# Kernel optimization log

Measured on AMD Instinct MI355X. Metric: run time of the kernel, lower is better.

## Reference

```python
import jax, jax.numpy as jnp
import numpy as np

B, T, LATENT, D, N_ENVS = 128, 64, 16, 512, 4
TOPK_RATIO = 0.1
TEMPERATURE = 1.0


def setup_inputs() -> dict:
    key = jax.random.key(0)
    k1, k2, k3, k4 = jax.random.split(key, 4)
    z_s = jax.random.normal(k1, (B, T, LATENT), dtype=jnp.float32)
    env_idx = jax.random.randint(k2, (B,), 0, N_ENVS, dtype=jnp.int64 if jax.config.jax_enable_x64 else jnp.int32)
    A_base = jax.random.normal(k3, (D, D), dtype=jnp.float32) * 0.1
    A_deltas = jax.random.normal(k4, (N_ENVS, D, D), dtype=jnp.float32) * 0.01  # stacked ParameterList
    return {"z_s": z_s, "env_idx": env_idx, "A_base": A_base, "A_deltas": A_deltas}


def reference(z_s, env_idx, A_base, A_deltas):
    b = z_s.shape[0]
    d = A_base.shape[0]
    # Per-env delta add: the torch loop sums delta_e * (env_idx==e) over envs,
    # which (one env per sample) equals a gather of A_deltas at env_idx.
    A_logits = A_base[None, :, :] + A_deltas[env_idx]          # [B, d, d]
    A_soft = jax.nn.sigmoid(A_logits / TEMPERATURE)            # [B, d, d]
    # Batched top-k sparsification (replaces the per-sample python loop).
    k = max(1, int(TOPK_RATIO * d * d))
    flat = A_logits.reshape(b, d * d)                          # [B, d*d]
    topk_vals, topk_idx = jax.lax.top_k(flat, k)               # [B, k]
    rows = jnp.arange(b)[:, None]                              # [B, 1]
    A_flat = jnp.zeros_like(flat).at[rows, topk_idx].set(jax.nn.sigmoid(topk_vals))
    A = A_flat.reshape(b, d, d)
    return A, A_logits, A_soft
```

## Files before the change

### kernel.cpp

```cpp
#include <hip/hip_runtime.h>
#include <stdint.h>

#define D_DIM   512
#define DD      262144
#define DD4     65536
#define B_DIM   128
#define N_ENVS  4
#define K_SEL   26214
#define BDD     33554432u
#define NBLK    64
#define CAP2    98304
#define CAP3    4096

typedef float nfloat4 __attribute__((ext_vector_type(4)));

#define PK_OFF      64
#define CNT_OFF     128
#define HISTP_OFF   4096
#define PAIRS_OFF   (512 * 1024)
#define PAIRS_BYTES ((size_t)N_ENVS * CAP2 * 8)
#define SEL_NEED    (PAIRS_OFF + PAIRS_BYTES)

__device__ __forceinline__ uint32_t fkey(float f) {
    uint32_t u = __float_as_uint(f);
    return (u & 0x80000000u) ? ~u : (u | 0x80000000u);
}
__device__ __forceinline__ float sigmoidf_(float x) {
    return 1.0f / (1.0f + __expf(-x));
}

__global__ __launch_bounds__(256) void hist8_kernel(
    const float* __restrict__ base, const float* __restrict__ deltas,
    uint32_t* __restrict__ histp, uint32_t* __restrict__ cnt8)
{
    int e = blockIdx.y;
    const float4* b4 = (const float4*)base;
    const float4* d4 = (const float4*)(deltas + (size_t)e * DD);
    __shared__ uint32_t s_h[256];
    int tid = threadIdx.x;
    s_h[tid] = 0;
    if (blockIdx.x == 0 && tid == 0) cnt8[e] = 0;
    __syncthreads();
    int g0 = blockIdx.x * 256 + tid;
    #pragma unroll
    for (int r = 0; r < 4; ++r) {
        int g = g0 + r * 16384;
        float4 bv = b4[g], dv = d4[g];
        atomicAdd(&s_h[fkey(bv.x + dv.x) >> 24], 1u);
        atomicAdd(&s_h[fkey(bv.y + dv.y) >> 24], 1u);
        atomicAdd(&s_h[fkey(bv.z + dv.z) >> 24], 1u);
        atomicAdd(&s_h[fkey(bv.w + dv.w) >> 24], 1u);
    }
    __syncthreads();
    histp[(blockIdx.x * N_ENVS + e) * 256 + tid] = s_h[tid];
}

__global__ __launch_bounds__(256) void gather8_kernel(
    const float* __restrict__ base, const float* __restrict__ deltas,
    const uint32_t* __restrict__ histp, uint32_t* __restrict__ pk,
    uint32_t* __restrict__ cnt8, uint2* __restrict__ pairs8)
{
    int e = blockIdx.y;
    const float4* b4 = (const float4*)base;
    const float4* d4 = (const float4*)(deltas + (size_t)e * DD);
    uint2* pp = pairs8 + (size_t)e * CAP2;
    __shared__ uint32_t s_h[256];
    __shared__ uint32_t s_scan[256];
    __shared__ uint32_t s_P, s_base;
    int tid = threadIdx.x;

    uint32_t sum = 0;
    #pragma unroll 8
    for (int j = 0; j < NBLK; ++j)
        sum += histp[(j * N_ENVS + e) * 256 + tid];
    s_h[tid] = sum;
    __syncthreads();
    if (tid == 0) {
        uint32_t cum = 0;
        for (int b = 255; b >= 0; --b) {
            uint32_t c = s_h[b];
            if (cum + c >= (uint32_t)K_SEL) {
                s_P = (uint32_t)b;
                if (blockIdx.x == 0) {
                    pk[2 * e + 0] = (uint32_t)b;
                    pk[2 * e + 1] = (uint32_t)K_SEL - cum;
                }
                break;
            }
            cum += c;
        }
    }
    __syncthreads();
    uint32_t P = s_P;

    int g0 = blockIdx.x * 256 + tid;
    uint32_t keys[16];
    uint32_t m = 0;
    #pragma unroll
    for (int r = 0; r < 4; ++r) {
        int g = g0 + r * 16384;
        float4 bv = b4[g], dv = d4[g];
        uint32_t k0 = fkey(bv.x + dv.x), k1 = fkey(bv.y + dv.y);
        uint32_t k2 = fkey(bv.z + dv.z), k3 = fkey(bv.w + dv.w);
        keys[r * 4 + 0] = k0; keys[r * 4 + 1] = k1;
        keys[r * 4 + 2] = k2; keys[r * 4 + 3] = k3;
        m += ((k0 >> 24) == P) + ((k1 >> 24) == P)
           + ((k2 >> 24) == P) + ((k3 >> 24) == P);
    }
    s_scan[tid] = m;
    __syncthreads();
    #pragma unroll
    for (int off = 1; off < 256; off <<= 1) {
        uint32_t v = (tid >= off) ? s_scan[tid - off] : 0u;
        __syncthreads();
        s_scan[tid] += v;
        __syncthreads();
    }
    uint32_t excl = s_scan[tid] - m;
    if (tid == 255) s_base = atomicAdd(&cnt8[e], s_scan[255]);
    __syncthreads();
    uint32_t pos = s_base + excl;

    #pragma unroll
    for (int r = 0; r < 4; ++r) {
        int g = g0 + r * 16384;
        #pragma unroll
        for (int j = 0; j < 4; ++j) {
            uint32_t key = keys[r * 4 + j];
            if ((key >> 24) == P) {
                if (pos < CAP2) pp[pos] = make_uint2(key, (uint32_t)(g * 4 + j));
                ++pos;
            }
        }
    }
}

__global__ __launch_bounds__(1024) void select2_kernel(
    const uint32_t* __restrict__ pk, const uint32_t* __restrict__ cnt8,
    const uint2* __restrict__ pairs8, uint32_t* __restrict__ thrcut)
{
    int e = blockIdx.x;
    const uint2* pp = pairs8 + (size_t)e * CAP2;
    uint32_t M = cnt8[e]; if (M > CAP2) M = CAP2;
    uint32_t krem8 = pk[2 * e + 1];

    __shared__ uint32_t s_h16[256];
    __shared__ uint2    s_pairs[CAP3];
    __shared__ uint32_t s_b16, s_krem16, s_cnt;
    int tid = threadIdx.x;
    if (tid < 256) s_h16[tid] = 0;
    if (tid == 0) s_cnt = 0;
    __syncthreads();

    for (uint32_t j = tid; j < M; j += 1024)
        atomicAdd(&s_h16[(pp[j].x >> 16) & 255u], 1u);
    __syncthreads();
    if (tid == 0) {
        uint32_t cum = 0;
        for (int b = 255; b >= 0; --b) {
            uint32_t c = s_h16[b];
            if (cum + c >= krem8) { s_b16 = (uint32_t)b; s_krem16 = krem8 - cum; break; }
            cum += c;
        }
    }
    __syncthreads();
    uint32_t b16 = s_b16;
    for (uint32_t j = tid; j < M; j += 1024) {
        uint2 p = pp[j];
        if (((p.x >> 16) & 255u) == b16) {
            uint32_t pos = atomicAdd(&s_cnt, 1u);
            if (pos < CAP3) s_pairs[pos] = p;
        }
    }
    __syncthreads();
    uint32_t M2 = s_cnt; if (M2 > CAP3) M2 = CAP3;
    uint32_t target = s_krem16 - 1;
    for (uint32_t j = tid; j < M2; j += 1024) {
        uint2 me = s_pairs[j];
        uint32_t rank = 0;
        for (uint32_t l = 0; l < M2; ++l) {
            uint2 o = s_pairs[l];
            rank += (o.x > me.x) || (o.x == me.x && o.y < me.y);
        }
        if (rank == target) {
            thrcut[2 * e + 0] = me.x;
            thrcut[2 * e + 1] = me.y;
        }
    }
}

__global__ __launch_bounds__(256) void write_bcast_kernel(
    const int* __restrict__ env_idx, const float* __restrict__ base,
    const float* __restrict__ deltas, const uint32_t* __restrict__ thrcut,
    float* __restrict__ out)
{
    int g = blockIdx.x * 256 + threadIdx.x;
    uint32_t i0 = (uint32_t)g * 4u;
    float4 bv = ((const float4*)base)[g];

    nfloat4 lgv[N_ENVS], sgv[N_ENVS], avv[N_ENVS];
    #pragma unroll
    for (int e = 0; e < N_ENVS; ++e) {
        float4 dv = ((const float4*)(deltas + (size_t)e * DD))[g];
        uint32_t T = thrcut[2 * e], C = thrcut[2 * e + 1];
        nfloat4 lg = { bv.x + dv.x, bv.y + dv.y, bv.z + dv.z, bv.w + dv.w };
        nfloat4 sg = { sigmoidf_(lg.x), sigmoidf_(lg.y),
                       sigmoidf_(lg.z), sigmoidf_(lg.w) };
        uint32_t kx = fkey(lg.x), ky = fkey(lg.y);
        uint32_t kz = fkey(lg.z), kw = fkey(lg.w);
        nfloat4 av;
        av.x = (kx > T || (kx == T && i0 + 0u <= C)) ? sg.x : 0.0f;
        av.y = (ky > T || (ky == T && i0 + 1u <= C)) ? sg.y : 0.0f;
        av.z = (kz > T || (kz == T && i0 + 2u <= C)) ? sg.z : 0.0f;
        av.w = (kw > T || (kw == T && i0 + 3u <= C)) ? sg.w : 0.0f;
        lgv[e] = lg; sgv[e] = sg; avv[e] = av;
    }

    const int ROWS = B_DIM / 8;
    int b0 = blockIdx.y * ROWS;
    nfloat4* o0 = (nfloat4*)out + g;
    #pragma unroll 4
    for (int bb = 0; bb < ROWS; ++bb) {
        int b = b0 + bb;
        int e = env_idx[b];
        nfloat4* o = o0 + (size_t)b * DD4;
        switch (e) {
        case 0: o[0] = avv[0]; o[BDD/4] = lgv[0]; o[2*(BDD/4)] = sgv[0]; break;
        case 1: o[0] = avv[1]; o[BDD/4] = lgv[1]; o[2*(BDD/4)] = sgv[1]; break;
        case 2: o[0] = avv[2]; o[BDD/4] = lgv[2]; o[2*(BDD/4)] = sgv[2]; break;
        default: o[0] = avv[3]; o[BDD/4] = lgv[3]; o[2*(BDD/4)] = sgv[3]; break;
        }
    }
}

extern "C" void kernel_launch(void* const* d_in, const int* in_sizes, int n_in,
                              void* d_out, int out_size, void* d_ws, size_t ws_size,
                              hipStream_t stream) {
    const int*   env_idx  = (const int*)d_in[1];
    const float* A_base   = (const float*)d_in[2];
    const float* A_deltas = (const float*)d_in[3];
    float* out = (float*)d_out;

    uint32_t* thrcut = (uint32_t*)d_ws;

    char* scratch;
    if (ws_size >= SEL_NEED) {
        scratch = (char*)d_ws;
    } else {
        size_t out_bytes = (size_t)out_size * sizeof(float);
        scratch = (char*)d_out + ((out_bytes - SEL_NEED) & ~(size_t)255);
    }
    uint32_t* pk     = (uint32_t*)(scratch + PK_OFF);
    uint32_t* cnt8   = (uint32_t*)(scratch + CNT_OFF);
    uint32_t* histp  = (uint32_t*)(scratch + HISTP_OFF);
    uint2*    pairs8 = (uint2*)   (scratch + PAIRS_OFF);

    hist8_kernel  <<<dim3(NBLK, N_ENVS), 256, 0, stream>>>(A_base, A_deltas,
                                                           histp, cnt8);
    gather8_kernel<<<dim3(NBLK, N_ENVS), 256, 0, stream>>>(A_base, A_deltas, histp,
                                                           pk, cnt8, pairs8);
    select2_kernel<<<N_ENVS, 1024, 0, stream>>>(pk, cnt8, pairs8, thrcut);
    write_bcast_kernel<<<dim3(DD4 / 256, 8), 256, 0, stream>>>(
        env_idx, A_base, A_deltas, thrcut, out);
}
```

Measured before the change: 456.3 us.

## Fuse top-k pipeline into one cooperative kernel with early logit/sigmoid writes

Replaces the four-kernel sequence (histogram, gather, select, broadcast write) with a single cooperative kernel that uses grid-wide syncs between phases. The logits and sigmoid output writes, which are two thirds of the output traffic, are moved ahead of the threshold selection so they overlap the radix-select work. Only the sparse A output is written after the threshold is known. This removes launch gaps between kernels, but during the select phase only 4 of 256 blocks are busy. The write phase also has fewer, larger threads than the old broadcast kernel. The old path remains as a fallback if the cooperative launch fails or the workspace is too small.

```diff
diff --git a/kernel.cpp b/kernel.cpp
--- a/kernel.cpp
+++ b/kernel.cpp
@@ -1,5 +1,8 @@
 #include <hip/hip_runtime.h>
+#include <hip/hip_cooperative_groups.h>
 #include <stdint.h>
+
+namespace cg = cooperative_groups;
 
 #define D_DIM   512
 #define DD      262144
@@ -8,6 +11,7 @@
 #define N_ENVS  4
 #define K_SEL   26214
 #define BDD     33554432u
+#define NSLICE  64
 #define NBLK    64
 #define CAP2    98304
 #define CAP3    4096
@@ -27,6 +31,205 @@
 }
 __device__ __forceinline__ float sigmoidf_(float x) {
     return 1.0f / (1.0f + __expf(-x));
+}
+
+__global__ __launch_bounds__(1024) void mega_kernel(
+    const int* __restrict__ env_idx, const float* __restrict__ base,
+    const float* __restrict__ deltas, uint32_t* __restrict__ histp,
+    uint32_t* __restrict__ cnt8, uint2* __restrict__ pairs8,
+    uint32_t* __restrict__ thrcut, float* __restrict__ out)
+{
+    cg::grid_group grid = cg::this_grid();
+    const int bid = blockIdx.x;
+    const int tid = threadIdx.x;
+    const int e   = bid & (N_ENVS - 1);
+    const int s   = bid >> 2;
+
+    __shared__ uint32_t s_h[256];
+    __shared__ uint32_t s_scan[1024];
+    __shared__ uint32_t s_misc[4];
+    __shared__ uint2    s_pairs[CAP3];
+
+    const float4* b4 = (const float4*)base;
+    const float4* d4 = (const float4*)(deltas + (size_t)e * DD);
+
+    if (tid < 256) s_h[tid] = 0;
+    if (s == 0 && tid == 0) cnt8[e] = 0;
+    __syncthreads();
+    const int g_sel = s * 1024 + tid;
+    float4 bs = b4[g_sel], ds = d4[g_sel];
+    uint32_t k0 = fkey(bs.x + ds.x), k1 = fkey(bs.y + ds.y);
+    uint32_t k2 = fkey(bs.z + ds.z), k3 = fkey(bs.w + ds.w);
+    atomicAdd(&s_h[k0 >> 24], 1u);
+    atomicAdd(&s_h[k1 >> 24], 1u);
+    atomicAdd(&s_h[k2 >> 24], 1u);
+    atomicAdd(&s_h[k3 >> 24], 1u);
+    __syncthreads();
+    if (tid < 256) histp[(s * N_ENVS + e) * 256 + tid] = s_h[tid];
+
+    {
+        const int gt = bid * 1024 + tid;
+        const int gq = gt & (DD4 - 1);
+        const int h  = gt >> 16;
+        float4 bq = b4[gq];
+        nfloat4 lgv[N_ENVS], sgv[N_ENVS];
+        #pragma unroll
+        for (int e2 = 0; e2 < N_ENVS; ++e2) {
+            float4 dq = ((const float4*)(deltas + (size_t)e2 * DD))[gq];
+            nfloat4 lg = { bq.x + dq.x, bq.y + dq.y, bq.z + dq.z, bq.w + dq.w };
+            lgv[e2] = lg;
+            sgv[e2] = nfloat4{ sigmoidf_(lg.x), sigmoidf_(lg.y),
+                               sigmoidf_(lg.z), sigmoidf_(lg.w) };
+        }
+        nfloat4* o0 = (nfloat4*)out + gq;
+        #pragma unroll 4
+        for (int bb = 0; bb < 32; ++bb) {
+            int b = h * 32 + bb;
+            int ee = env_idx[b];
+            nfloat4* o = o0 + (size_t)b * DD4;
+            switch (ee) {
+            case 0:  o[BDD/4] = lgv[0]; o[2*(BDD/4)] = sgv[0]; break;
+            case 1:  o[BDD/4] = lgv[1]; o[2*(BDD/4)] = sgv[1]; break;
+            case 2:  o[BDD/4] = lgv[2]; o[2*(BDD/4)] = sgv[2]; break;
+            default: o[BDD/4] = lgv[3]; o[2*(BDD/4)] = sgv[3]; break;
+            }
+        }
+    }
+    grid.sync();
+
+    if (tid < 256) {
+        uint32_t sum = 0;
+        #pragma unroll 8
+        for (int j = 0; j < NSLICE; ++j)
+            sum += histp[(j * N_ENVS + e) * 256 + tid];
+        s_h[tid] = sum;
+    }
+    __syncthreads();
+    if (tid == 0) {
+        uint32_t cum = 0;
+        for (int b = 255; b >= 0; --b) {
+            uint32_t c = s_h[b];
+            if (cum + c >= (uint32_t)K_SEL) {
+                s_misc[0] = (uint32_t)b;
+                s_misc[1] = (uint32_t)K_SEL - cum;
+                break;
+            }
+            cum += c;
+        }
+    }
+    __syncthreads();
+    const uint32_t P = s_misc[0];
+    uint32_t m = ((k0 >> 24) == P) + ((k1 >> 24) == P)
+               + ((k2 >> 24) == P) + ((k3 >> 24) == P);
+    s_scan[tid] = m;
+    __syncthreads();
+    #pragma unroll
+    for (int off = 1; off < 1024; off <<= 1) {
+        uint32_t v = (tid >= off) ? s_scan[tid - off] : 0u;
+        __syncthreads();
+        s_scan[tid] += v;
+        __syncthreads();
+    }
+    uint32_t excl = s_scan[tid] - m;
+    if (tid == 1023) s_misc[2] = atomicAdd(&cnt8[e], s_scan[1023]);
+    __syncthreads();
+    {
+        uint32_t pos = s_misc[2] + excl;
+        uint2* pp = pairs8 + (size_t)e * CAP2;
+        uint32_t kk[4] = { k0, k1, k2, k3 };
+        #pragma unroll
+        for (int j = 0; j < 4; ++j) {
+            if ((kk[j] >> 24) == P) {
+                if (pos < CAP2) pp[pos] = make_uint2(kk[j], (uint32_t)(g_sel * 4 + j));
+                ++pos;
+            }
+        }
+    }
+    grid.sync();
+
+    if (bid < N_ENVS) {
+        const uint2* pp = pairs8 + (size_t)bid * CAP2;
+        uint32_t M = cnt8[bid]; if (M > CAP2) M = CAP2;
+        uint32_t krem8 = s_misc[1];
+        if (tid < 256) s_h[tid] = 0;
+        if (tid == 0) s_misc[3] = 0;
+        __syncthreads();
+        for (uint32_t j = tid; j < M; j += 1024)
+            atomicAdd(&s_h[(pp[j].x >> 16) & 255u], 1u);
+        __syncthreads();
+        if (tid == 0) {
+            uint32_t cum = 0;
+            for (int b = 255; b >= 0; --b) {
+                uint32_t c = s_h[b];
+                if (cum + c >= krem8) { s_misc[0] = (uint32_t)b; s_misc[1] = krem8 - cum; break; }
+                cum += c;
+            }
+        }
+        __syncthreads();
+        uint32_t b16 = s_misc[0];
+        for (uint32_t j = tid; j < M; j += 1024) {
+            uint2 p = pp[j];
+            if (((p.x >> 16) & 255u) == b16) {
+                uint32_t pos = atomicAdd(&s_misc[3], 1u);
+                if (pos < CAP3) s_pairs[pos] = p;
+            }
+        }
+        __syncthreads();
+        uint32_t M2 = s_misc[3]; if (M2 > CAP3) M2 = CAP3;
+        uint32_t target = s_misc[1] - 1;
+        for (uint32_t j = tid; j < M2; j += 1024) {
+            uint2 me = s_pairs[j];
+            uint32_t rank = 0;
+            for (uint32_t l = 0; l < M2; ++l) {
+                uint2 o = s_pairs[l];
+                rank += (o.x > me.x) || (o.x == me.x && o.y < me.y);
+            }
+            if (rank == target) {
+                thrcut[2 * bid + 0] = me.x;
+                thrcut[2 * bid + 1] = me.y;
+            }
+        }
+        __threadfence();
+    }
+    grid.sync();
+
+    {
+        const int gt = bid * 1024 + tid;
+        const int gq = gt & (DD4 - 1);
+        const int h  = gt >> 16;
+        const uint32_t i0 = (uint32_t)gq * 4u;
+        float4 bq = b4[gq];
+        nfloat4 avv[N_ENVS];
+        #pragma unroll
+        for (int e2 = 0; e2 < N_ENVS; ++e2) {
+            float4 dq = ((const float4*)(deltas + (size_t)e2 * DD))[gq];
+            uint32_t T = thrcut[2 * e2], C = thrcut[2 * e2 + 1];
+            nfloat4 lg = { bq.x + dq.x, bq.y + dq.y, bq.z + dq.z, bq.w + dq.w };
+            nfloat4 sg = { sigmoidf_(lg.x), sigmoidf_(lg.y),
+                           sigmoidf_(lg.z), sigmoidf_(lg.w) };
+            uint32_t kx = fkey(lg.x), ky = fkey(lg.y);
+            uint32_t kz = fkey(lg.z), kw = fkey(lg.w);
+            nfloat4 av;
+            av.x = (kx > T || (kx == T && i0 + 0u <= C)) ? sg.x : 0.0f;
+            av.y = (ky > T || (ky == T && i0 + 1u <= C)) ? sg.y : 0.0f;
+            av.z = (kz > T || (kz == T && i0 + 2u <= C)) ? sg.z : 0.0f;
+            av.w = (kw > T || (kw == T && i0 + 3u <= C)) ? sg.w : 0.0f;
+            avv[e2] = av;
+        }
+        nfloat4* o0 = (nfloat4*)out + gq;
+        #pragma unroll 4
+        for (int bb = 0; bb < 32; ++bb) {
+            int b = h * 32 + bb;
+            int ee = env_idx[b];
+            nfloat4* o = o0 + (size_t)b * DD4;
+            switch (ee) {
+            case 0:  o[0] = avv[0]; break;
+            case 1:  o[0] = avv[1]; break;
+            case 2:  o[0] = avv[2]; break;
+            default: o[0] = avv[3]; break;
+            }
+        }
+    }
 }
 
 __global__ __launch_bounds__(256) void hist8_kernel(
@@ -68,7 +271,6 @@
     __shared__ uint32_t s_scan[256];
     __shared__ uint32_t s_P, s_base;
     int tid = threadIdx.x;
-
     uint32_t sum = 0;
     #pragma unroll 8
     for (int j = 0; j < NBLK; ++j)
@@ -92,7 +294,6 @@
     }
     __syncthreads();
     uint32_t P = s_P;
-
     int g0 = blockIdx.x * 256 + tid;
     uint32_t keys[16];
     uint32_t m = 0;
@@ -100,12 +301,10 @@
     for (int r = 0; r < 4; ++r) {
         int g = g0 + r * 16384;
         float4 bv = b4[g], dv = d4[g];
-        uint32_t k0 = fkey(bv.x + dv.x), k1 = fkey(bv.y + dv.y);
-        uint32_t k2 = fkey(bv.z + dv.z), k3 = fkey(bv.w + dv.w);
-        keys[r * 4 + 0] = k0; keys[r * 4 + 1] = k1;
-        keys[r * 4 + 2] = k2; keys[r * 4 + 3] = k3;
-        m += ((k0 >> 24) == P) + ((k1 >> 24) == P)
-           + ((k2 >> 24) == P) + ((k3 >> 24) == P);
+        uint32_t c0 = fkey(bv.x + dv.x), c1 = fkey(bv.y + dv.y);
+        uint32_t c2 = fkey(bv.z + dv.z), c3 = fkey(bv.w + dv.w);
+        keys[r*4+0]=c0; keys[r*4+1]=c1; keys[r*4+2]=c2; keys[r*4+3]=c3;
+        m += ((c0>>24)==P) + ((c1>>24)==P) + ((c2>>24)==P) + ((c3>>24)==P);
     }
     s_scan[tid] = m;
     __syncthreads();
@@ -120,7 +319,6 @@
     if (tid == 255) s_base = atomicAdd(&cnt8[e], s_scan[255]);
     __syncthreads();
     uint32_t pos = s_base + excl;
-
     #pragma unroll
     for (int r = 0; r < 4; ++r) {
         int g = g0 + r * 16384;
@@ -143,7 +341,6 @@
     const uint2* pp = pairs8 + (size_t)e * CAP2;
     uint32_t M = cnt8[e]; if (M > CAP2) M = CAP2;
     uint32_t krem8 = pk[2 * e + 1];
-
     __shared__ uint32_t s_h16[256];
     __shared__ uint2    s_pairs[CAP3];
     __shared__ uint32_t s_b16, s_krem16, s_cnt;
@@ -151,7 +348,6 @@
     if (tid < 256) s_h16[tid] = 0;
     if (tid == 0) s_cnt = 0;
     __syncthreads();
-
     for (uint32_t j = tid; j < M; j += 1024)
         atomicAdd(&s_h16[(pp[j].x >> 16) & 255u], 1u);
     __syncthreads();
@@ -197,7 +393,6 @@
     int g = blockIdx.x * 256 + threadIdx.x;
     uint32_t i0 = (uint32_t)g * 4u;
     float4 bv = ((const float4*)base)[g];
-
     nfloat4 lgv[N_ENVS], sgv[N_ENVS], avv[N_ENVS];
     #pragma unroll
     for (int e = 0; e < N_ENVS; ++e) {
@@ -215,7 +410,6 @@
         av.w = (kw > T || (kw == T && i0 + 3u <= C)) ? sg.w : 0.0f;
         lgv[e] = lg; sgv[e] = sg; avv[e] = av;
     }
-
     const int ROWS = B_DIM / 8;
     int b0 = blockIdx.y * ROWS;
     nfloat4* o0 = (nfloat4*)out + g;
@@ -243,8 +437,9 @@
 
     uint32_t* thrcut = (uint32_t*)d_ws;
 
+    bool ws_ok = (ws_size >= SEL_NEED);
     char* scratch;
-    if (ws_size >= SEL_NEED) {
+    if (ws_ok) {
         scratch = (char*)d_ws;
     } else {
         size_t out_bytes = (size_t)out_size * sizeof(float);
@@ -255,11 +450,24 @@
     uint32_t* histp  = (uint32_t*)(scratch + HISTP_OFF);
     uint2*    pairs8 = (uint2*)   (scratch + PAIRS_OFF);
 
-    hist8_kernel  <<<dim3(NBLK, N_ENVS), 256, 0, stream>>>(A_base, A_deltas,
-                                                           histp, cnt8);
-    gather8_kernel<<<dim3(NBLK, N_ENVS), 256, 0, stream>>>(A_base, A_deltas, histp,
-                                                           pk, cnt8, pairs8);
-    select2_kernel<<<N_ENVS, 1024, 0, stream>>>(pk, cnt8, pairs8, thrcut);
-    write_bcast_kernel<<<dim3(DD4 / 256, 8), 256, 0, stream>>>(
-        env_idx, A_base, A_deltas, thrcut, out);
-}
+    bool launched = false;
+    if (ws_ok) {
+        void* args[] = { (void*)&env_idx, (void*)&A_base, (void*)&A_deltas,
+                         (void*)&histp, (void*)&cnt8, (void*)&pairs8,
+                         (void*)&thrcut, (void*)&out };
+        hipError_t err = hipLaunchCooperativeKernel(
+            (const void*)mega_kernel, dim3(NSLICE * N_ENVS), dim3(1024),
+            args, 0, stream);
+        launched = (err == hipSuccess);
+        if (!launched) (void)hipGetLastError();
+    }
+    if (!launched) {
+        hist8_kernel  <<<dim3(NBLK, N_ENVS), 256, 0, stream>>>(A_base, A_deltas,
+                                                               histp, cnt8);
+        gather8_kernel<<<dim3(NBLK, N_ENVS), 256, 0, stream>>>(A_base, A_deltas,
+                                                               histp, pk, cnt8, pairs8);
+        select2_kernel<<<N_ENVS, 1024, 0, stream>>>(pk, cnt8, pairs8, thrcut);
+        write_bcast_kernel<<<dim3(DD4 / 256, 8), 256, 0, stream>>>(
+            env_idx, A_base, A_deltas, thrcut, out);
+    }
+}
```

Result: slower. 556.7 us (+22.0%).

## Fuse select pass into gather kernel via last-block ticket, cache env_idx in LDS

Applied to the files above, without the earlier changes.

Removes the separate select2 launch. The last block to finish the gather kernel (found with an atomic ticket counter plus threadfences) now does the per-env radix refinement and rank selection for all four envs in sequence. It uses 256 threads instead of four 1024-thread blocks. The write kernel also stages env_idx in shared memory. This saves one kernel launch and its gap, but the selection tail now runs serially on a single block with a quarter of the threads, so it may take longer.

```diff
diff --git a/kernel.cpp b/kernel.cpp
--- a/kernel.cpp
+++ b/kernel.cpp
@@ -16,6 +16,7 @@
 
 #define PK_OFF      64
 #define CNT_OFF     128
+#define TICKET_OFF  144
 #define HISTP_OFF   4096
 #define PAIRS_OFF   (512 * 1024)
 #define PAIRS_BYTES ((size_t)N_ENVS * CAP2 * 8)
@@ -31,7 +32,8 @@
 
 __global__ __launch_bounds__(256) void hist8_kernel(
     const float* __restrict__ base, const float* __restrict__ deltas,
-    uint32_t* __restrict__ histp, uint32_t* __restrict__ cnt8)
+    uint32_t* __restrict__ histp, uint32_t* __restrict__ cnt8,
+    uint32_t* __restrict__ ticket)
 {
     int e = blockIdx.y;
     const float4* b4 = (const float4*)base;
@@ -39,7 +41,10 @@
     __shared__ uint32_t s_h[256];
     int tid = threadIdx.x;
     s_h[tid] = 0;
-    if (blockIdx.x == 0 && tid == 0) cnt8[e] = 0;
+    if (blockIdx.x == 0 && tid == 0) {
+        cnt8[e] = 0;
+        if (e == 0) *ticket = 0;
+    }
     __syncthreads();
     int g0 = blockIdx.x * 256 + tid;
     #pragma unroll
@@ -55,10 +60,11 @@
     histp[(blockIdx.x * N_ENVS + e) * 256 + tid] = s_h[tid];
 }
 
-__global__ __launch_bounds__(256) void gather8_kernel(
+__global__ __launch_bounds__(256) void gather_sel_kernel(
     const float* __restrict__ base, const float* __restrict__ deltas,
     const uint32_t* __restrict__ histp, uint32_t* __restrict__ pk,
-    uint32_t* __restrict__ cnt8, uint2* __restrict__ pairs8)
+    uint32_t* __restrict__ cnt8, uint2* __restrict__ pairs8,
+    uint32_t* __restrict__ ticket, uint32_t* __restrict__ thrcut)
 {
     int e = blockIdx.y;
     const float4* b4 = (const float4*)base;
@@ -66,7 +72,8 @@
     uint2* pp = pairs8 + (size_t)e * CAP2;
     __shared__ uint32_t s_h[256];
     __shared__ uint32_t s_scan[256];
-    __shared__ uint32_t s_P, s_base;
+    __shared__ uint2    s_pairs[CAP3];
+    __shared__ uint32_t s_P, s_base, s_cnt, s_b16, s_krem16, s_last;
     int tid = threadIdx.x;
 
     uint32_t sum = 0;
@@ -100,12 +107,10 @@
     for (int r = 0; r < 4; ++r) {
         int g = g0 + r * 16384;
         float4 bv = b4[g], dv = d4[g];
-        uint32_t k0 = fkey(bv.x + dv.x), k1 = fkey(bv.y + dv.y);
-        uint32_t k2 = fkey(bv.z + dv.z), k3 = fkey(bv.w + dv.w);
-        keys[r * 4 + 0] = k0; keys[r * 4 + 1] = k1;
-        keys[r * 4 + 2] = k2; keys[r * 4 + 3] = k3;
-        m += ((k0 >> 24) == P) + ((k1 >> 24) == P)
-           + ((k2 >> 24) == P) + ((k3 >> 24) == P);
+        uint32_t c0 = fkey(bv.x + dv.x), c1 = fkey(bv.y + dv.y);
+        uint32_t c2 = fkey(bv.z + dv.z), c3 = fkey(bv.w + dv.w);
+        keys[r*4+0]=c0; keys[r*4+1]=c1; keys[r*4+2]=c2; keys[r*4+3]=c3;
+        m += ((c0>>24)==P) + ((c1>>24)==P) + ((c2>>24)==P) + ((c3>>24)==P);
     }
     s_scan[tid] = m;
     __syncthreads();
@@ -133,59 +138,59 @@
             }
         }
     }
-}
-
-__global__ __launch_bounds__(1024) void select2_kernel(
-    const uint32_t* __restrict__ pk, const uint32_t* __restrict__ cnt8,
-    const uint2* __restrict__ pairs8, uint32_t* __restrict__ thrcut)
-{
-    int e = blockIdx.x;
-    const uint2* pp = pairs8 + (size_t)e * CAP2;
-    uint32_t M = cnt8[e]; if (M > CAP2) M = CAP2;
-    uint32_t krem8 = pk[2 * e + 1];
-
-    __shared__ uint32_t s_h16[256];
-    __shared__ uint2    s_pairs[CAP3];
-    __shared__ uint32_t s_b16, s_krem16, s_cnt;
-    int tid = threadIdx.x;
-    if (tid < 256) s_h16[tid] = 0;
-    if (tid == 0) s_cnt = 0;
-    __syncthreads();
-
-    for (uint32_t j = tid; j < M; j += 1024)
-        atomicAdd(&s_h16[(pp[j].x >> 16) & 255u], 1u);
-    __syncthreads();
-    if (tid == 0) {
-        uint32_t cum = 0;
-        for (int b = 255; b >= 0; --b) {
-            uint32_t c = s_h16[b];
-            if (cum + c >= krem8) { s_b16 = (uint32_t)b; s_krem16 = krem8 - cum; break; }
-            cum += c;
-        }
-    }
-    __syncthreads();
-    uint32_t b16 = s_b16;
-    for (uint32_t j = tid; j < M; j += 1024) {
-        uint2 p = pp[j];
-        if (((p.x >> 16) & 255u) == b16) {
-            uint32_t pos = atomicAdd(&s_cnt, 1u);
-            if (pos < CAP3) s_pairs[pos] = p;
-        }
-    }
-    __syncthreads();
-    uint32_t M2 = s_cnt; if (M2 > CAP3) M2 = CAP3;
-    uint32_t target = s_krem16 - 1;
-    for (uint32_t j = tid; j < M2; j += 1024) {
-        uint2 me = s_pairs[j];
-        uint32_t rank = 0;
-        for (uint32_t l = 0; l < M2; ++l) {
-            uint2 o = s_pairs[l];
-            rank += (o.x > me.x) || (o.x == me.x && o.y < me.y);
-        }
-        if (rank == target) {
-            thrcut[2 * e + 0] = me.x;
-            thrcut[2 * e + 1] = me.y;
-        }
+
+    __threadfence();
+    __syncthreads();
+    if (tid == 0)
+        s_last = (atomicAdd(ticket, 1u) == (uint32_t)(NBLK * N_ENVS - 1));
+    __syncthreads();
+    if (!s_last) return;
+    __threadfence();
+
+    for (int e2 = 0; e2 < N_ENVS; ++e2) {
+        const uint2* qq = pairs8 + (size_t)e2 * CAP2;
+        uint32_t M = cnt8[e2]; if (M > CAP2) M = CAP2;
+        uint32_t krem8 = pk[2 * e2 + 1];
+
+        s_h[tid] = 0;
+        if (tid == 0) s_cnt = 0;
+        __syncthreads();
+        for (uint32_t j = tid; j < M; j += 256)
+            atomicAdd(&s_h[(qq[j].x >> 16) & 255u], 1u);
+        __syncthreads();
+        if (tid == 0) {
+            uint32_t cum = 0;
+            for (int b = 255; b >= 0; --b) {
+                uint32_t c = s_h[b];
+                if (cum + c >= krem8) { s_b16 = (uint32_t)b; s_krem16 = krem8 - cum; break; }
+                cum += c;
+            }
+        }
+        __syncthreads();
+        uint32_t b16 = s_b16;
+        for (uint32_t j = tid; j < M; j += 256) {
+            uint2 p = qq[j];
+            if (((p.x >> 16) & 255u) == b16) {
+                uint32_t q = atomicAdd(&s_cnt, 1u);
+                if (q < CAP3) s_pairs[q] = p;
+            }
+        }
+        __syncthreads();
+        uint32_t M2 = s_cnt; if (M2 > CAP3) M2 = CAP3;
+        uint32_t target = s_krem16 - 1;
+        for (uint32_t j = tid; j < M2; j += 256) {
+            uint2 me = s_pairs[j];
+            uint32_t rank = 0;
+            for (uint32_t l = 0; l < M2; ++l) {
+                uint2 o = s_pairs[l];
+                rank += (o.x > me.x) || (o.x == me.x && o.y < me.y);
+            }
+            if (rank == target) {
+                thrcut[2 * e2 + 0] = me.x;
+                thrcut[2 * e2 + 1] = me.y;
+            }
+        }
+        __syncthreads();
     }
 }
 
@@ -194,7 +199,11 @@
     const float* __restrict__ deltas, const uint32_t* __restrict__ thrcut,
     float* __restrict__ out)
 {
-    int g = blockIdx.x * 256 + threadIdx.x;
+    __shared__ int s_env[B_DIM];
+    int tid = threadIdx.x;
+    if (tid < B_DIM) s_env[tid] = env_idx[tid];
+
+    int g = blockIdx.x * 256 + tid;
     uint32_t i0 = (uint32_t)g * 4u;
     float4 bv = ((const float4*)base)[g];
 
@@ -215,6 +224,7 @@
         av.w = (kw > T || (kw == T && i0 + 3u <= C)) ? sg.w : 0.0f;
         lgv[e] = lg; sgv[e] = sg; avv[e] = av;
     }
+    __syncthreads();
 
     const int ROWS = B_DIM / 8;
     int b0 = blockIdx.y * ROWS;
@@ -222,7 +232,7 @@
     #pragma unroll 4
     for (int bb = 0; bb < ROWS; ++bb) {
         int b = b0 + bb;
-        int e = env_idx[b];
+        int e = s_env[b];
         nfloat4* o = o0 + (size_t)b * DD4;
         switch (e) {
         case 0: o[0] = avv[0]; o[BDD/4] = lgv[0]; o[2*(BDD/4)] = sgv[0]; break;
@@ -252,14 +262,14 @@
     }
     uint32_t* pk     = (uint32_t*)(scratch + PK_OFF);
     uint32_t* cnt8   = (uint32_t*)(scratch + CNT_OFF);
+    uint32_t* ticket = (uint32_t*)(scratch + TICKET_OFF);
     uint32_t* histp  = (uint32_t*)(scratch + HISTP_OFF);
     uint2*    pairs8 = (uint2*)   (scratch + PAIRS_OFF);
 
-    hist8_kernel  <<<dim3(NBLK, N_ENVS), 256, 0, stream>>>(A_base, A_deltas,
-                                                           histp, cnt8);
-    gather8_kernel<<<dim3(NBLK, N_ENVS), 256, 0, stream>>>(A_base, A_deltas, histp,
-                                                           pk, cnt8, pairs8);
-    select2_kernel<<<N_ENVS, 1024, 0, stream>>>(pk, cnt8, pairs8, thrcut);
+    hist8_kernel<<<dim3(NBLK, N_ENVS), 256, 0, stream>>>(
+        A_base, A_deltas, histp, cnt8, ticket);
+    gather_sel_kernel<<<dim3(NBLK, N_ENVS), 256, 0, stream>>>(
+        A_base, A_deltas, histp, pk, cnt8, pairs8, ticket, thrcut);
     write_bcast_kernel<<<dim3(DD4 / 256, 8), 256, 0, stream>>>(
         env_idx, A_base, A_deltas, thrcut, out);
 }
```

New measurement: 793.1 us. 1.74x slower.

## Overlap logits/sigmoid plane writes with top-k selection kernels

Applied to the files above, without the earlier changes.

Adds extra blocks to the histogram and gather kernels that write the A_logits and A_soft output planes, so those bandwidth-heavy stores run while the latency-bound selection stages work. The final kernel then writes only the sparse A plane. Env indices are staged in shared memory. When the workspace is too small, the old path is kept, because scratch then aliases the output buffer. The risk is extra contention in the selection kernels, but the total bytes written stay the same.

```diff
diff --git a/kernel.cpp b/kernel.cpp
--- a/kernel.cpp
+++ b/kernel.cpp
@@ -21,6 +21,9 @@
 #define PAIRS_BYTES ((size_t)N_ENVS * CAP2 * 8)
 #define SEL_NEED    (PAIRS_OFF + PAIRS_BYTES)
 
+#define SEL_BLOCKS  (NBLK * N_ENVS)
+#define WR_BLOCKS   1024
+
 __device__ __forceinline__ uint32_t fkey(float f) {
     uint32_t u = __float_as_uint(f);
     return (u & 0x80000000u) ? ~u : (u | 0x80000000u);
@@ -29,109 +32,161 @@
     return 1.0f / (1.0f + __expf(-x));
 }
 
-__global__ __launch_bounds__(256) void hist8_kernel(
-    const float* __restrict__ base, const float* __restrict__ deltas,
-    uint32_t* __restrict__ histp, uint32_t* __restrict__ cnt8)
-{
-    int e = blockIdx.y;
-    const float4* b4 = (const float4*)base;
-    const float4* d4 = (const float4*)(deltas + (size_t)e * DD);
-    __shared__ uint32_t s_h[256];
-    int tid = threadIdx.x;
-    s_h[tid] = 0;
-    if (blockIdx.x == 0 && tid == 0) cnt8[e] = 0;
-    __syncthreads();
-    int g0 = blockIdx.x * 256 + tid;
+__device__ __forceinline__ void write_lgsg_band(
+    const int* __restrict__ env_idx, const float* __restrict__ base,
+    const float* __restrict__ deltas, float* __restrict__ out,
+    int c, int h, int tid)
+{
+    __shared__ int s_env[16];
+    if (tid < 16) s_env[tid] = env_idx[h * 16 + tid];
+    int g = c * 256 + tid;
+    float4 bv = ((const float4*)base)[g];
+    nfloat4 lgv[N_ENVS], sgv[N_ENVS];
     #pragma unroll
-    for (int r = 0; r < 4; ++r) {
-        int g = g0 + r * 16384;
-        float4 bv = b4[g], dv = d4[g];
-        atomicAdd(&s_h[fkey(bv.x + dv.x) >> 24], 1u);
-        atomicAdd(&s_h[fkey(bv.y + dv.y) >> 24], 1u);
-        atomicAdd(&s_h[fkey(bv.z + dv.z) >> 24], 1u);
-        atomicAdd(&s_h[fkey(bv.w + dv.w) >> 24], 1u);
-    }
-    __syncthreads();
-    histp[(blockIdx.x * N_ENVS + e) * 256 + tid] = s_h[tid];
-}
-
-__global__ __launch_bounds__(256) void gather8_kernel(
-    const float* __restrict__ base, const float* __restrict__ deltas,
-    const uint32_t* __restrict__ histp, uint32_t* __restrict__ pk,
-    uint32_t* __restrict__ cnt8, uint2* __restrict__ pairs8)
-{
-    int e = blockIdx.y;
-    const float4* b4 = (const float4*)base;
-    const float4* d4 = (const float4*)(deltas + (size_t)e * DD);
-    uint2* pp = pairs8 + (size_t)e * CAP2;
-    __shared__ uint32_t s_h[256];
-    __shared__ uint32_t s_scan[256];
-    __shared__ uint32_t s_P, s_base;
-    int tid = threadIdx.x;
-
-    uint32_t sum = 0;
-    #pragma unroll 8
-    for (int j = 0; j < NBLK; ++j)
-        sum += histp[(j * N_ENVS + e) * 256 + tid];
-    s_h[tid] = sum;
-    __syncthreads();
-    if (tid == 0) {
-        uint32_t cum = 0;
-        for (int b = 255; b >= 0; --b) {
-            uint32_t c = s_h[b];
-            if (cum + c >= (uint32_t)K_SEL) {
-                s_P = (uint32_t)b;
-                if (blockIdx.x == 0) {
-                    pk[2 * e + 0] = (uint32_t)b;
-                    pk[2 * e + 1] = (uint32_t)K_SEL - cum;
+    for (int e = 0; e < N_ENVS; ++e) {
+        float4 dv = ((const float4*)(deltas + (size_t)e * DD))[g];
+        nfloat4 lg = { bv.x + dv.x, bv.y + dv.y, bv.z + dv.z, bv.w + dv.w };
+        lgv[e] = lg;
+        sgv[e] = nfloat4{ sigmoidf_(lg.x), sigmoidf_(lg.y),
+                          sigmoidf_(lg.z), sigmoidf_(lg.w) };
+    }
+    __syncthreads();
+    nfloat4* o0 = (nfloat4*)out + g;
+    #pragma unroll 4
+    for (int bb = 0; bb < 16; ++bb) {
+        int b = h * 16 + bb;
+        int e = s_env[bb];
+        nfloat4* o = o0 + (size_t)b * DD4;
+        switch (e) {
+        case 0:  o[BDD/4] = lgv[0]; o[2*(BDD/4)] = sgv[0]; break;
+        case 1:  o[BDD/4] = lgv[1]; o[2*(BDD/4)] = sgv[1]; break;
+        case 2:  o[BDD/4] = lgv[2]; o[2*(BDD/4)] = sgv[2]; break;
+        default: o[BDD/4] = lgv[3]; o[2*(BDD/4)] = sgv[3]; break;
+        }
+    }
+}
+
+__global__ __launch_bounds__(256) void k1_hist_lgsg(
+    const int* __restrict__ env_idx, const float* __restrict__ base,
+    const float* __restrict__ deltas, uint32_t* __restrict__ histp,
+    uint32_t* __restrict__ cnt8, float* __restrict__ out)
+{
+    int bid = blockIdx.x;
+    int tid = threadIdx.x;
+    if (bid < SEL_BLOCKS) {
+        int e = bid & (N_ENVS - 1);
+        int s = bid >> 2;
+        const float4* b4 = (const float4*)base;
+        const float4* d4 = (const float4*)(deltas + (size_t)e * DD);
+        __shared__ uint32_t s_h[256];
+        s_h[tid] = 0;
+        if (s == 0 && tid == 0) cnt8[e] = 0;
+        __syncthreads();
+        int g0 = s * 256 + tid;
+        #pragma unroll
+        for (int r = 0; r < 4; ++r) {
+            int g = g0 + r * 16384;
+            float4 bv = b4[g], dv = d4[g];
+            atomicAdd(&s_h[fkey(bv.x + dv.x) >> 24], 1u);
+            atomicAdd(&s_h[fkey(bv.y + dv.y) >> 24], 1u);
+            atomicAdd(&s_h[fkey(bv.z + dv.z) >> 24], 1u);
+            atomicAdd(&s_h[fkey(bv.w + dv.w) >> 24], 1u);
+        }
+        __syncthreads();
+        histp[(s * N_ENVS + e) * 256 + tid] = s_h[tid];
+    } else {
+        int w = bid - SEL_BLOCKS;
+        int c = w & 255;
+        int h = w >> 8;
+        write_lgsg_band(env_idx, base, deltas, out, c, h, tid);
+    }
+}
+
+__global__ __launch_bounds__(256) void k2_gather_lgsg(
+    const int* __restrict__ env_idx, const float* __restrict__ base,
+    const float* __restrict__ deltas, const uint32_t* __restrict__ histp,
+    uint32_t* __restrict__ pk, uint32_t* __restrict__ cnt8,
+    uint2* __restrict__ pairs8, float* __restrict__ out)
+{
+    int bid = blockIdx.x;
+    int tid = threadIdx.x;
+    if (bid < SEL_BLOCKS) {
+        int e = bid & (N_ENVS - 1);
+        int s = bid >> 2;
+        const float4* b4 = (const float4*)base;
+        const float4* d4 = (const float4*)(deltas + (size_t)e * DD);
+        uint2* pp = pairs8 + (size_t)e * CAP2;
+        __shared__ uint32_t s_h[256];
+        __shared__ uint32_t s_scan[256];
+        __shared__ uint32_t s_P, s_base;
+
+        uint32_t sum = 0;
+        #pragma unroll 8
+        for (int j = 0; j < NBLK; ++j)
+            sum += histp[(j * N_ENVS + e) * 256 + tid];
+        s_h[tid] = sum;
+        __syncthreads();
+        if (tid == 0) {
+            uint32_t cum = 0;
+            for (int b = 255; b >= 0; --b) {
+                uint32_t cc = s_h[b];
+                if (cum + cc >= (uint32_t)K_SEL) {
+                    s_P = (uint32_t)b;
+                    if (s == 0) {
+                        pk[2 * e + 0] = (uint32_t)b;
+                        pk[2 * e + 1] = (uint32_t)K_SEL - cum;
+                    }
+                    break;
                 }
-                break;
+                cum += cc;
             }
-            cum += c;
-        }
-    }
-    __syncthreads();
-    uint32_t P = s_P;
-
-    int g0 = blockIdx.x * 256 + tid;
-    uint32_t keys[16];
-    uint32_t m = 0;
-    #pragma unroll
-    for (int r = 0; r < 4; ++r) {
-        int g = g0 + r * 16384;
-        float4 bv = b4[g], dv = d4[g];
-        uint32_t k0 = fkey(bv.x + dv.x), k1 = fkey(bv.y + dv.y);
-        uint32_t k2 = fkey(bv.z + dv.z), k3 = fkey(bv.w + dv.w);
-        keys[r * 4 + 0] = k0; keys[r * 4 + 1] = k1;
-        keys[r * 4 + 2] = k2; keys[r * 4 + 3] = k3;
-        m += ((k0 >> 24) == P) + ((k1 >> 24) == P)
-           + ((k2 >> 24) == P) + ((k3 >> 24) == P);
-    }
-    s_scan[tid] = m;
-    __syncthreads();
-    #pragma unroll
-    for (int off = 1; off < 256; off <<= 1) {
-        uint32_t v = (tid >= off) ? s_scan[tid - off] : 0u;
-        __syncthreads();
-        s_scan[tid] += v;
-        __syncthreads();
-    }
-    uint32_t excl = s_scan[tid] - m;
-    if (tid == 255) s_base = atomicAdd(&cnt8[e], s_scan[255]);
-    __syncthreads();
-    uint32_t pos = s_base + excl;
-
-    #pragma unroll
-    for (int r = 0; r < 4; ++r) {
-        int g = g0 + r * 16384;
+        }
+        __syncthreads();
+        uint32_t P = s_P;
+
+        int g0 = s * 256 + tid;
+        uint32_t keys[16];
+        uint32_t m = 0;
         #pragma unroll
-        for (int j = 0; j < 4; ++j) {
-            uint32_t key = keys[r * 4 + j];
-            if ((key >> 24) == P) {
-                if (pos < CAP2) pp[pos] = make_uint2(key, (uint32_t)(g * 4 + j));
-                ++pos;
+        for (int r = 0; r < 4; ++r) {
+            int g = g0 + r * 16384;
+            float4 bv = b4[g], dv = d4[g];
+            uint32_t c0 = fkey(bv.x + dv.x), c1 = fkey(bv.y + dv.y);
+            uint32_t c2 = fkey(bv.z + dv.z), c3 = fkey(bv.w + dv.w);
+            keys[r*4+0]=c0; keys[r*4+1]=c1; keys[r*4+2]=c2; keys[r*4+3]=c3;
+            m += ((c0>>24)==P) + ((c1>>24)==P) + ((c2>>24)==P) + ((c3>>24)==P);
+        }
+        s_scan[tid] = m;
+        __syncthreads();
+        #pragma unroll
+        for (int off = 1; off < 256; off <<= 1) {
+            uint32_t v = (tid >= off) ? s_scan[tid - off] : 0u;
+            __syncthreads();
+            s_scan[tid] += v;
+            __syncthreads();
+        }
+        uint32_t excl = s_scan[tid] - m;
+        if (tid == 255) s_base = atomicAdd(&cnt8[e], s_scan[255]);
+        __syncthreads();
+        uint32_t pos = s_base + excl;
+
+        #pragma unroll
+        for (int r = 0; r < 4; ++r) {
+            int g = g0 + r * 16384;
+            #pragma unroll
+            for (int j = 0; j < 4; ++j) {
+                uint32_t key = keys[r * 4 + j];
+                if ((key >> 24) == P) {
+                    if (pos < CAP2) pp[pos] = make_uint2(key, (uint32_t)(g * 4 + j));
+                    ++pos;
+                }
             }
         }
+    } else {
+        int w = bid - SEL_BLOCKS;
+        int c = w & 255;
+        int h = 4 + (w >> 8);
+        write_lgsg_band(env_idx, base, deltas, out, c, h, tid);
     }
 }
 
@@ -143,7 +198,6 @@
     const uint2* pp = pairs8 + (size_t)e * CAP2;
     uint32_t M = cnt8[e]; if (M > CAP2) M = CAP2;
     uint32_t krem8 = pk[2 * e + 1];
-
     __shared__ uint32_t s_h16[256];
     __shared__ uint2    s_pairs[CAP3];
     __shared__ uint32_t s_b16, s_krem16, s_cnt;
@@ -151,7 +205,6 @@
     if (tid < 256) s_h16[tid] = 0;
     if (tid == 0) s_cnt = 0;
     __syncthreads();
-
     for (uint32_t j = tid; j < M; j += 1024)
         atomicAdd(&s_h16[(pp[j].x >> 16) & 255u], 1u);
     __syncthreads();
@@ -189,15 +242,62 @@
     }
 }
 
-__global__ __launch_bounds__(256) void write_bcast_kernel(
+__global__ __launch_bounds__(256) void k4_aplane(
     const int* __restrict__ env_idx, const float* __restrict__ base,
     const float* __restrict__ deltas, const uint32_t* __restrict__ thrcut,
     float* __restrict__ out)
 {
-    int g = blockIdx.x * 256 + threadIdx.x;
+    __shared__ int s_env[16];
+    int tid = threadIdx.x;
+    int h = blockIdx.y;
+    if (tid < 16) s_env[tid] = env_idx[h * 16 + tid];
+    int g = blockIdx.x * 256 + tid;
     uint32_t i0 = (uint32_t)g * 4u;
     float4 bv = ((const float4*)base)[g];
-
+    nfloat4 avv[N_ENVS];
+    #pragma unroll
+    for (int e = 0; e < N_ENVS; ++e) {
+        float4 dv = ((const float4*)(deltas + (size_t)e * DD))[g];
+        uint32_t T = thrcut[2 * e], C = thrcut[2 * e + 1];
+        nfloat4 lg = { bv.x + dv.x, bv.y + dv.y, bv.z + dv.z, bv.w + dv.w };
+        nfloat4 sg = { sigmoidf_(lg.x), sigmoidf_(lg.y),
+                       sigmoidf_(lg.z), sigmoidf_(lg.w) };
+        uint32_t kx = fkey(lg.x), ky = fkey(lg.y);
+        uint32_t kz = fkey(lg.z), kw = fkey(lg.w);
+        nfloat4 av;
+        av.x = (kx > T || (kx == T && i0 + 0u <= C)) ? sg.x : 0.0f;
+        av.y = (ky > T || (ky == T && i0 + 1u <= C)) ? sg.y : 0.0f;
+        av.z = (kz > T || (kz == T && i0 + 2u <= C)) ? sg.z : 0.0f;
+        av.w = (kw > T || (kw == T && i0 + 3u <= C)) ? sg.w : 0.0f;
+        avv[e] = av;
+    }
+    __syncthreads();
+    nfloat4* o0 = (nfloat4*)out + g;
+    #pragma unroll 4
+    for (int bb = 0; bb < 16; ++bb) {
+        int b = h * 16 + bb;
+        int e = s_env[bb];
+        nfloat4* o = o0 + (size_t)b * DD4;
+        switch (e) {
+        case 0:  o[0] = avv[0]; break;
+        case 1:  o[0] = avv[1]; break;
+        case 2:  o[0] = avv[2]; break;
+        default: o[0] = avv[3]; break;
+        }
+    }
+}
+
+__global__ __launch_bounds__(256) void write_bcast_kernel(
+    const int* __restrict__ env_idx, const float* __restrict__ base,
+    const float* __restrict__ deltas, const uint32_t* __restrict__ thrcut,
+    float* __restrict__ out)
+{
+    __shared__ int s_env[B_DIM];
+    int tid = threadIdx.x;
+    if (tid < B_DIM) s_env[tid] = env_idx[tid];
+    int g = blockIdx.x * 256 + tid;
+    uint32_t i0 = (uint32_t)g * 4u;
+    float4 bv = ((const float4*)base)[g];
     nfloat4 lgv[N_ENVS], sgv[N_ENVS], avv[N_ENVS];
     #pragma unroll
     for (int e = 0; e < N_ENVS; ++e) {
@@ -215,14 +315,14 @@
         av.w = (kw > T || (kw == T && i0 + 3u <= C)) ? sg.w : 0.0f;
         lgv[e] = lg; sgv[e] = sg; avv[e] = av;
     }
-
+    __syncthreads();
     const int ROWS = B_DIM / 8;
     int b0 = blockIdx.y * ROWS;
     nfloat4* o0 = (nfloat4*)out + g;
     #pragma unroll 4
     for (int bb = 0; bb < ROWS; ++bb) {
         int b = b0 + bb;
-        int e = env_idx[b];
+        int e = s_env[b];
         nfloat4* o = o0 + (size_t)b * DD4;
         switch (e) {
         case 0: o[0] = avv[0]; o[BDD/4] = lgv[0]; o[2*(BDD/4)] = sgv[0]; break;
@@ -243,8 +343,9 @@
 
     uint32_t* thrcut = (uint32_t*)d_ws;
 
+    bool ws_ok = (ws_size >= SEL_NEED);
     char* scratch;
-    if (ws_size >= SEL_NEED) {
+    if (ws_ok) {
         scratch = (char*)d_ws;
     } else {
         size_t out_bytes = (size_t)out_size * sizeof(float);
@@ -255,11 +356,21 @@
     uint32_t* histp  = (uint32_t*)(scratch + HISTP_OFF);
     uint2*    pairs8 = (uint2*)   (scratch + PAIRS_OFF);
 
-    hist8_kernel  <<<dim3(NBLK, N_ENVS), 256, 0, stream>>>(A_base, A_deltas,
-                                                           histp, cnt8);
-    gather8_kernel<<<dim3(NBLK, N_ENVS), 256, 0, stream>>>(A_base, A_deltas, histp,
-                                                           pk, cnt8, pairs8);
-    select2_kernel<<<N_ENVS, 1024, 0, stream>>>(pk, cnt8, pairs8, thrcut);
-    write_bcast_kernel<<<dim3(DD4 / 256, 8), 256, 0, stream>>>(
-        env_idx, A_base, A_deltas, thrcut, out);
-}
+    if (ws_ok) {
+        k1_hist_lgsg<<<SEL_BLOCKS + WR_BLOCKS, 256, 0, stream>>>(
+            env_idx, A_base, A_deltas, histp, cnt8, out);
+        k2_gather_lgsg<<<SEL_BLOCKS + WR_BLOCKS, 256, 0, stream>>>(
+            env_idx, A_base, A_deltas, histp, pk, cnt8, pairs8, out);
+        select2_kernel<<<N_ENVS, 1024, 0, stream>>>(pk, cnt8, pairs8, thrcut);
+        k4_aplane<<<dim3(256, 8), 256, 0, stream>>>(
+            env_idx, A_base, A_deltas, thrcut, out);
+    } else {
+        k1_hist_lgsg<<<SEL_BLOCKS, 256, 0, stream>>>(
+            env_idx, A_base, A_deltas, histp, cnt8, out);
+        k2_gather_lgsg<<<SEL_BLOCKS, 256, 0, stream>>>(
+            env_idx, A_base, A_deltas, histp, pk, cnt8, pairs8, out);
+        select2_kernel<<<N_ENVS, 1024, 0, stream>>>(pk, cnt8, pairs8, thrcut);
+        write_bcast_kernel<<<dim3(256, 8), 256, 0, stream>>>(
+            env_idx, A_base, A_deltas, thrcut, out);
+    }
+}
```

Result: faster. 446.7 us (-2.1%).
